# Kernel tuning notes

Hardware: AMD Instinct MI355X
Metric: run time of the kernel (lower is better)

Reference implementation:

```python
import jax, jax.numpy as jnp
import numpy as np

IMG = 800          # original image H = W
OUT = 7            # pooled output size
SR = 2             # sampling_ratio
CANON_S = 224.0    # canonical_scale
CANON_L = 4.0      # canonical_level
EPS = 1e-6
KMIN, KMAX = 2, 5  # -log2 of first/last scale


def _bilinear_gather(feat, b_idx, y, x):
    """feat: [B,C,H,W]; b_idx: [N] int; y,x: [N,S] float sample coords.
    Returns [N,S,C]. Faithful to torchvision roi_align bilinear_interpolate
    (aligned=False semantics)."""
    B, C, H, W = feat.shape
    valid = (y > -1.0) & (y < H) & (x > -1.0) & (x < W)
    y = jnp.clip(y, 0.0, None)
    x = jnp.clip(x, 0.0, None)
    yl = jnp.minimum(jnp.floor(y).astype(jnp.int32), H - 1)
    xl = jnp.minimum(jnp.floor(x).astype(jnp.int32), W - 1)
    yh = jnp.minimum(yl + 1, H - 1)
    xh = jnp.minimum(xl + 1, W - 1)
    y = jnp.where(yl >= H - 1, yl.astype(y.dtype), y)
    x = jnp.where(xl >= W - 1, xl.astype(x.dtype), x)
    ly = y - yl
    lx = x - xl
    hy = 1.0 - ly
    hx = 1.0 - lx
    flat = feat.transpose(0, 2, 3, 1).reshape(B * H * W, C)  # [B*H*W, C]
    base = b_idx[:, None] * (H * W)                            # [N,1]

    def g(yy, xx):
        return flat[base + yy * W + xx]  # gather -> [N,S,C]

    val = ((hy * hx)[..., None] * g(yl, xl)
           + (hy * lx)[..., None] * g(yl, xh)
           + (ly * hx)[..., None] * g(yh, xl)
           + (ly * lx)[..., None] * g(yh, xh))
    return jnp.where(valid[..., None], val, 0.0)


def _roi_align(feat, rois, scale):
    """Single-level RoIAlign, aligned=False. rois: [N,5] = (batch_idx,x1,y1,x2,y2)."""
    N = rois.shape[0]
    C = feat.shape[1]
    b_idx = rois[:, 0].astype(jnp.int32)
    x1 = rois[:, 1] * scale
    y1 = rois[:, 2] * scale
    x2 = rois[:, 3] * scale
    y2 = rois[:, 4] * scale
    roi_w = jnp.maximum(x2 - x1, 1.0)
    roi_h = jnp.maximum(y2 - y1, 1.0)
    bin_w = roi_w / OUT
    bin_h = roi_h / OUT
    # sample offsets within the roi, in units of bins: [OUT*SR]
    off = (jnp.arange(OUT, dtype=feat.dtype)[:, None]
           + (jnp.arange(SR, dtype=feat.dtype)[None, :] + 0.5) / SR).reshape(-1)
    ys = y1[:, None] + off[None, :] * bin_h[:, None]  # [N, OUT*SR]
    xs = x1[:, None] + off[None, :] * bin_w[:, None]  # [N, OUT*SR]
    S = OUT * SR
    Y = jnp.broadcast_to(ys[:, :, None], (N, S, S)).reshape(N, S * S)
    X = jnp.broadcast_to(xs[:, None, :], (N, S, S)).reshape(N, S * S)
    val = _bilinear_gather(feat, b_idx, Y, X)          # [N, S*S, C]
    val = val.reshape(N, OUT, SR, OUT, SR, C).mean(axis=(2, 4))  # avg over samples
    return val.transpose(0, 3, 1, 2)                   # [N, C, OUT, OUT]


def setup_inputs() -> dict:
    key = jax.random.key(0)
    ks = jax.random.split(key, 7)
    feats = {}
    for i, hw in enumerate([200, 100, 50, 25]):
        feats[f"feat{i}"] = jax.random.normal(ks[i], (2, 256, hw, hw), dtype=jnp.float32)
    # boxes [2, 256, 4] in (x1,y1,x2,y2), sizes log-uniform in [16, ~590] px
    xy1 = jax.random.uniform(ks[4], (2, 256, 2), minval=0.0, maxval=IMG - 32.0)
    sz = 2.0 ** jax.random.uniform(ks[5], (2, 256, 2), minval=4.0, maxval=9.2)
    xy2 = jnp.minimum(xy1 + sz, float(IMG))
    boxes = jnp.concatenate([xy1, xy2], axis=-1).astype(jnp.float32)
    return {**feats, "boxes": boxes}


def reference(feat0, feat1, feat2, feat3, boxes):
    feats = [feat0, feat1, feat2, feat3]
    # _infer_scale: round(log2(feat_size / image_size)) -> power-of-two scale
    scales = [2.0 ** round(float(np.log2(f.shape[2] / IMG))) for f in feats]
    # _convert_to_roi_format
    B, Nb, _ = boxes.shape
    ids = jnp.repeat(jnp.arange(B, dtype=boxes.dtype), Nb)[:, None]
    rois = jnp.concatenate([ids, boxes.reshape(B * Nb, 4)], axis=1)  # [N,5]
    # LevelMapper (FPN eq.1)
    s = jnp.sqrt((rois[:, 3] - rois[:, 1]) * (rois[:, 4] - rois[:, 2]))
    lvls = jnp.floor(CANON_L + jnp.log2(s / CANON_S) + EPS)
    lvls = jnp.clip(lvls, KMIN, KMAX).astype(jnp.int32) - KMIN  # [N] in {0..3}
    out = jnp.zeros((B * Nb, feat0.shape[1], OUT, OUT), dtype=feat0.dtype)
    for lvl, (f, sc) in enumerate(zip(feats, scales)):
        r = _roi_align(f, rois, sc)
        out = jnp.where((lvls == lvl)[:, None, None, None], r, out)
    return out
```

## Files before the change

kernel.cpp:

```cpp
#include <hip/hip_runtime.h>
#include <hip/hip_bf16.h>


#define IMGC   256
#define OUTP   7
#define NBIN   49
#define SAMP   14
#define BT     128
#define TLD    132
#define SLD    68

#define WS_O1 20480000
#define WS_O2 25600000
#define WS_O3 26880000
#define WS_TOT 27200000

__global__ __launch_bounds__(256) void transpose_cl_kernel(
    const float* __restrict__ f0, const float* __restrict__ f1,
    const float* __restrict__ f2, const float* __restrict__ f3,
    float* __restrict__ ws)
{
    __shared__ float t[64 * SLD];

    int bx = blockIdx.x;
    int lvl, r;
    if (bx < 5000)      { lvl = 0; r = bx; }
    else if (bx < 6256) { lvl = 1; r = bx - 5000; }
    else if (bx < 6576) { lvl = 2; r = bx - 6256; }
    else                { lvl = 3; r = bx - 6576; }

    const int  Mtab[4]  = {40000, 10000, 2500, 625};
    const int  Mttab[4] = {625, 157, 40, 10};
    const int  wsoff[4] = {0, WS_O1, WS_O2, WS_O3};

    const float* in = (lvl == 0) ? f0 : (lvl == 1) ? f1 : (lvl == 2) ? f2 : f3;
    float* outp = ws + wsoff[lvl];
    const int M  = Mtab[lvl];
    const int Mt = Mttab[lvl];

    int mt   = r % Mt;
    int rest = r / Mt;
    int ct   = rest & 3;
    int bb   = rest >> 2;
    int m0   = mt * 64;

    const bool vec = (m0 + 64 <= M) && ((M & 3) == 0);

    if (vec) {
        int mq = threadIdx.x & 15;
        int cg = threadIdx.x >> 4;
        const float* ibase = in + (bb * IMGC + ct * 64) * M + m0;
        #pragma unroll
        for (int j = 0; j < 4; ++j) {
            int c = cg + 16 * j;
            float4 v = *(const float4*)(ibase + c * M + 4 * mq);
            *(float4*)&t[c * SLD + 4 * mq] = v;
        }
        __syncthreads();
        int cq = threadIdx.x & 15;
        int mr = threadIdx.x >> 4;
        float* obase = outp + (bb * M + m0) * IMGC + ct * 64;
        #pragma unroll
        for (int j = 0; j < 4; ++j) {
            int m = mr + 16 * j;
            float4 v;
            v.x = t[(4 * cq + 0) * SLD + m];
            v.y = t[(4 * cq + 1) * SLD + m];
            v.z = t[(4 * cq + 2) * SLD + m];
            v.w = t[(4 * cq + 3) * SLD + m];
            *(float4*)(obase + m * IMGC + 4 * cq) = v;
        }
    } else {
        int tx = threadIdx.x & 63;
        int tg = threadIdx.x >> 6;
        {
            int m = m0 + tx;
            if (m < M) {
                int base = (bb * IMGC + ct * 64) * M + m;
                #pragma unroll
                for (int k = 0; k < 16; ++k) {
                    int cc = tg * 16 + k;
                    t[cc * SLD + tx] = in[base + cc * M];
                }
            }
        }
        __syncthreads();
        #pragma unroll
        for (int k = 0; k < 16; ++k) {
            int mm = tg * 16 + k;
            int m = m0 + mm;
            if (m < M)
                outp[(bb * M + m) * IMGC + ct * 64 + tx] = t[tx * SLD + mm];
        }
    }
}

__global__ __launch_bounds__(BT) void roialign_cl_kernel(
    const float* __restrict__ f0, const float* __restrict__ f1,
    const float* __restrict__ f2, const float* __restrict__ f3,
    const float* __restrict__ boxes, float* __restrict__ out)
{
    __shared__ float  s_ly[SAMP], s_wy[SAMP], s_lx[SAMP], s_wx[SAMP];
    __shared__ int    s_yol[SAMP], s_yoh[SAMP], s_xol[SAMP], s_xoh[SAMP];
    __shared__ float4 s_w[SAMP * SAMP];
    __shared__ float  tile[NBIN * TLD];

    const int tid = threadIdx.x;
    const int blk = blockIdx.x;
    const int n   = blk >> 1;
    const int c0  = (blk & 1) * BT;
    const int b   = n >> 8;

    const float x1 = boxes[n * 4 + 0];
    const float y1 = boxes[n * 4 + 1];
    const float x2 = boxes[n * 4 + 2];
    const float y2 = boxes[n * 4 + 3];

    float s = sqrtf(fmaxf((x2 - x1) * (y2 - y1), 1e-12f));
    float lf = floorf(4.0f + log2f(s / 224.0f) + 1e-6f);
    int lvl = (int)fminf(fmaxf(lf, 2.0f), 5.0f) - 2;

    const int   Htab[4]  = {200, 100, 50, 25};
    const float sctab[4] = {0.25f, 0.125f, 0.0625f, 0.03125f};
    const int   H = Htab[lvl];
    const int   W = H;
    const float scale = sctab[lvl];
    const float* fp = (lvl == 0) ? f0 : (lvl == 1) ? f1 : (lvl == 2) ? f2 : f3;

    const float x1s = x1 * scale, y1s = y1 * scale;
    const float roi_w = fmaxf(x2 * scale - x1s, 1.0f);
    const float roi_h = fmaxf(y2 * scale - y1s, 1.0f);
    const float bin_w = roi_w * (1.0f / OUTP);
    const float bin_h = roi_h * (1.0f / OUTP);

    if (tid < SAMP) {
        int t = tid;
        float off = (float)(t >> 1) + 0.25f + 0.5f * (float)(t & 1);
        float y = y1s + off * bin_h;
        float v = (y > -1.0f && y < (float)H) ? 1.0f : 0.0f;
        y = fmaxf(y, 0.0f);
        int yl = min((int)y, H - 1);
        int yh = min(yl + 1, H - 1);
        if (yl >= H - 1) y = (float)yl;
        s_ly[t] = y - (float)yl;
        s_wy[t] = v;
        s_yol[t] = ((b * H + yl) * W) * (IMGC / 4);
        s_yoh[t] = ((b * H + yh) * W) * (IMGC / 4);
    } else if (tid >= 64 && tid < 64 + SAMP) {
        int t = tid - 64;
        float off = (float)(t >> 1) + 0.25f + 0.5f * (float)(t & 1);
        float x = x1s + off * bin_w;
        float v = (x > -1.0f && x < (float)W) ? 1.0f : 0.0f;
        x = fmaxf(x, 0.0f);
        int xl = min((int)x, W - 1);
        int xh = min(xl + 1, W - 1);
        if (xl >= W - 1) x = (float)xl;
        s_lx[t] = x - (float)xl;
        s_wx[t] = v;
        s_xol[t] = xl * (IMGC / 4);
        s_xoh[t] = xh * (IMGC / 4);
    }
    __syncthreads();

    for (int idx = tid; idx < SAMP * SAMP; idx += BT) {
        int i = idx / SAMP;
        int j = idx - i * SAMP;
        float v  = s_wy[i] * s_wx[j] * 0.25f;
        float ly = s_ly[i], lx = s_lx[j];
        float hy = 1.0f - ly, hx = 1.0f - lx;
        float4 w;
        w.x = v * hy * hx;
        w.y = v * hy * lx;
        w.z = v * ly * hx;
        w.w = v * ly * lx;
        s_w[idx] = w;
    }
    __syncthreads();

    const int quad = tid & 31;
    const int bg   = tid >> 5;
    const float4* fp4 = (const float4*)fp + (c0 / 4) + quad;

    for (int bin = bg; bin < NBIN; bin += 4) {
        int ph = bin / OUTP;
        int pw = bin - ph * OUTP;
        float4 acc; acc.x = acc.y = acc.z = acc.w = 0.0f;
        #pragma unroll
        for (int sy = 0; sy < 2; ++sy) {
            #pragma unroll
            for (int sx = 0; sx < 2; ++sx) {
                int i = 2 * ph + sy;
                int j = 2 * pw + sx;
                float4 w = s_w[i * SAMP + j];
                int yol = s_yol[i], yoh = s_yoh[i];
                int xol = s_xol[j], xoh = s_xoh[j];
                float4 v1 = fp4[yol + xol];
                float4 v2 = fp4[yol + xoh];
                float4 v3 = fp4[yoh + xol];
                float4 v4 = fp4[yoh + xoh];
                acc.x += w.x * v1.x + w.y * v2.x + w.z * v3.x + w.w * v4.x;
                acc.y += w.x * v1.y + w.y * v2.y + w.z * v3.y + w.w * v4.y;
                acc.z += w.x * v1.z + w.y * v2.z + w.z * v3.z + w.w * v4.z;
                acc.w += w.x * v1.w + w.y * v2.w + w.z * v3.w + w.w * v4.w;
            }
        }
        *(float4*)&tile[bin * TLD + 4 * quad] = acc;
    }
    __syncthreads();

    const int outbase = n * (IMGC * NBIN) + c0 * NBIN;
    for (int t = tid; t < BT * NBIN; t += BT) {
        int cl = t / NBIN;
        int bb = t - cl * NBIN;
        out[outbase + t] = tile[bb * TLD + cl];
    }
}

__global__ __launch_bounds__(BT) void roialign_direct_kernel(
    const float* __restrict__ f0, const float* __restrict__ f1,
    const float* __restrict__ f2, const float* __restrict__ f3,
    const float* __restrict__ boxes, float* __restrict__ out)
{
    __shared__ float s_ly[SAMP], s_wy[SAMP], s_lx[SAMP], s_wx[SAMP];
    __shared__ int   s_yol[SAMP], s_yoh[SAMP], s_xol[SAMP], s_xoh[SAMP];
    __shared__ float tile[NBIN * (BT + 1)];

    const int tid = threadIdx.x;
    const int blk = blockIdx.x;
    const int n   = blk >> 1;
    const int c0  = (blk & 1) * BT;
    const int b   = n >> 8;

    const float x1 = boxes[n * 4 + 0];
    const float y1 = boxes[n * 4 + 1];
    const float x2 = boxes[n * 4 + 2];
    const float y2 = boxes[n * 4 + 3];

    float s = sqrtf(fmaxf((x2 - x1) * (y2 - y1), 1e-12f));
    float lf = floorf(4.0f + log2f(s / 224.0f) + 1e-6f);
    int lvl = (int)fminf(fmaxf(lf, 2.0f), 5.0f) - 2;

    const int   Htab[4]  = {200, 100, 50, 25};
    const float sctab[4] = {0.25f, 0.125f, 0.0625f, 0.03125f};
    const int   H = Htab[lvl];
    const int   W = H;
    const float scale = sctab[lvl];
    const float* fp = (lvl == 0) ? f0 : (lvl == 1) ? f1 : (lvl == 2) ? f2 : f3;

    const float x1s = x1 * scale, y1s = y1 * scale;
    const float roi_w = fmaxf(x2 * scale - x1s, 1.0f);
    const float roi_h = fmaxf(y2 * scale - y1s, 1.0f);
    const float bin_w = roi_w * (1.0f / OUTP);
    const float bin_h = roi_h * (1.0f / OUTP);

    if (tid < SAMP) {
        int t = tid;
        float off = (float)(t >> 1) + 0.25f + 0.5f * (float)(t & 1);
        float y = y1s + off * bin_h;
        float v = (y > -1.0f && y < (float)H) ? 1.0f : 0.0f;
        y = fmaxf(y, 0.0f);
        int yl = min((int)y, H - 1);
        int yh = min(yl + 1, H - 1);
        if (yl >= H - 1) y = (float)yl;
        s_ly[t] = y - (float)yl;
        s_wy[t] = v;
        s_yol[t] = yl * W; s_yoh[t] = yh * W;
    } else if (tid >= 64 && tid < 64 + SAMP) {
        int t = tid - 64;
        float off = (float)(t >> 1) + 0.25f + 0.5f * (float)(t & 1);
        float x = x1s + off * bin_w;
        float v = (x > -1.0f && x < (float)W) ? 1.0f : 0.0f;
        x = fmaxf(x, 0.0f);
        int xl = min((int)x, W - 1);
        int xh = min(xl + 1, W - 1);
        if (xl >= W - 1) x = (float)xl;
        s_lx[t] = x - (float)xl;
        s_wx[t] = v;
        s_xol[t] = xl; s_xoh[t] = xh;
    }
    __syncthreads();

    const int c  = c0 + tid;
    const int tb = (b * IMGC + c) * (H * W);

    for (int bin = 0; bin < NBIN; ++bin) {
        int ph = bin / OUTP;
        int pw = bin - ph * OUTP;
        float acc = 0.0f;
        #pragma unroll
        for (int sy = 0; sy < 2; ++sy) {
            #pragma unroll
            for (int sx = 0; sx < 2; ++sx) {
                int i = 2 * ph + sy;
                int j = 2 * pw + sx;
                float ly = s_ly[i], lx = s_lx[j];
                float hy = 1.0f - ly, hx = 1.0f - lx;
                float wm = s_wy[i] * s_wx[j];
                float v1 = fp[tb + s_yol[i] + s_xol[j]];
                float v2 = fp[tb + s_yol[i] + s_xoh[j]];
                float v3 = fp[tb + s_yoh[i] + s_xol[j]];
                float v4 = fp[tb + s_yoh[i] + s_xoh[j]];
                acc += wm * (hy * (hx * v1 + lx * v2) + ly * (hx * v3 + lx * v4));
            }
        }
        tile[bin * (BT + 1) + tid] = acc * 0.25f;
    }
    __syncthreads();

    const int outbase = n * (IMGC * NBIN) + c0 * NBIN;
    for (int t = tid; t < BT * NBIN; t += BT) {
        int cl = t / NBIN;
        int bb = t - cl * NBIN;
        out[outbase + t] = tile[bb * (BT + 1) + cl];
    }
}

extern "C" void kernel_launch(void* const* d_in, const int* in_sizes, int n_in,
                              void* d_out, int out_size, void* d_ws, size_t ws_size,
                              hipStream_t stream) {
    const float* f0    = (const float*)d_in[0];
    const float* f1    = (const float*)d_in[1];
    const float* f2    = (const float*)d_in[2];
    const float* f3    = (const float*)d_in[3];
    const float* boxes = (const float*)d_in[4];
    float* out = (float*)d_out;

    const bool use_cl = ws_size >= (size_t)WS_TOT * sizeof(float);

    if (use_cl) {
        float* w = (float*)d_ws;
        transpose_cl_kernel<<<6656, 256, 0, stream>>>(f0, f1, f2, f3, w);
        roialign_cl_kernel<<<1024, BT, 0, stream>>>(
            w, w + WS_O1, w + WS_O2, w + WS_O3, boxes, out);
    } else {
        roialign_direct_kernel<<<1024, BT, 0, stream>>>(f0, f1, f2, f3, boxes, out);
    }
}
```

Before: 198.1 us.

## Store channels-last workspace in fp16 and gather half8 vectors in RoIAlign

The transpose kernel now writes the channels-last copy of each feature level as _Float16 instead of float. Each block handles all 256 channels of a 64-pixel tile through a larger, padded shared buffer with scalar loads. The RoIAlign kernel gathers half8 vectors, converts them to float and accumulates in fp32. This halves workspace write and gather traffic, at the cost of fp16 rounding of the features, which may exceed the accuracy tolerance. The transpose input reads are now scalar rather than float4.

```diff
diff --git a/kernel.cpp b/kernel.cpp
--- a/kernel.cpp
+++ b/kernel.cpp
@@ -8,97 +8,77 @@
 #define SAMP   14
 #define BT     128
 #define TLD    132
-#define SLD    68
+#define SLD    65
 
 #define WS_O1 20480000
 #define WS_O2 25600000
 #define WS_O3 26880000
 #define WS_TOT 27200000
 
-__global__ __launch_bounds__(256) void transpose_cl_kernel(
+typedef _Float16 half2v __attribute__((ext_vector_type(2)));
+typedef _Float16 half8  __attribute__((ext_vector_type(8)));
+
+__global__ __launch_bounds__(256) void transpose_cl_h_kernel(
     const float* __restrict__ f0, const float* __restrict__ f1,
     const float* __restrict__ f2, const float* __restrict__ f3,
-    float* __restrict__ ws)
+    _Float16* __restrict__ ws)
 {
-    __shared__ float t[64 * SLD];
+    __shared__ float t[IMGC * SLD];
 
     int bx = blockIdx.x;
     int lvl, r;
-    if (bx < 5000)      { lvl = 0; r = bx; }
-    else if (bx < 6256) { lvl = 1; r = bx - 5000; }
-    else if (bx < 6576) { lvl = 2; r = bx - 6256; }
-    else                { lvl = 3; r = bx - 6576; }
-
-    const int  Mtab[4]  = {40000, 10000, 2500, 625};
-    const int  Mttab[4] = {625, 157, 40, 10};
-    const int  wsoff[4] = {0, WS_O1, WS_O2, WS_O3};
+    if (bx < 1250)      { lvl = 0; r = bx; }
+    else if (bx < 1564) { lvl = 1; r = bx - 1250; }
+    else if (bx < 1644) { lvl = 2; r = bx - 1564; }
+    else                { lvl = 3; r = bx - 1644; }
+
+    const int Mtab[4]  = {40000, 10000, 2500, 625};
+    const int Mttab[4] = {625, 157, 40, 10};
+    const int wsoff[4] = {0, WS_O1, WS_O2, WS_O3};
 
     const float* in = (lvl == 0) ? f0 : (lvl == 1) ? f1 : (lvl == 2) ? f2 : f3;
-    float* outp = ws + wsoff[lvl];
+    _Float16* outp = ws + wsoff[lvl];
     const int M  = Mtab[lvl];
     const int Mt = Mttab[lvl];
 
-    int mt   = r % Mt;
-    int rest = r / Mt;
-    int ct   = rest & 3;
-    int bb   = rest >> 2;
-    int m0   = mt * 64;
-
-    const bool vec = (m0 + 64 <= M) && ((M & 3) == 0);
-
-    if (vec) {
-        int mq = threadIdx.x & 15;
-        int cg = threadIdx.x >> 4;
-        const float* ibase = in + (bb * IMGC + ct * 64) * M + m0;
-        #pragma unroll
-        for (int j = 0; j < 4; ++j) {
-            int c = cg + 16 * j;
-            float4 v = *(const float4*)(ibase + c * M + 4 * mq);
-            *(float4*)&t[c * SLD + 4 * mq] = v;
-        }
-        __syncthreads();
-        int cq = threadIdx.x & 15;
-        int mr = threadIdx.x >> 4;
-        float* obase = outp + (bb * M + m0) * IMGC + ct * 64;
-        #pragma unroll
-        for (int j = 0; j < 4; ++j) {
-            int m = mr + 16 * j;
-            float4 v;
-            v.x = t[(4 * cq + 0) * SLD + m];
-            v.y = t[(4 * cq + 1) * SLD + m];
-            v.z = t[(4 * cq + 2) * SLD + m];
-            v.w = t[(4 * cq + 3) * SLD + m];
-            *(float4*)(obase + m * IMGC + 4 * cq) = v;
-        }
-    } else {
-        int tx = threadIdx.x & 63;
-        int tg = threadIdx.x >> 6;
-        {
-            int m = m0 + tx;
-            if (m < M) {
-                int base = (bb * IMGC + ct * 64) * M + m;
-                #pragma unroll
-                for (int k = 0; k < 16; ++k) {
-                    int cc = tg * 16 + k;
-                    t[cc * SLD + tx] = in[base + cc * M];
-                }
+    int mt = r % Mt;
+    int bb = r / Mt;
+    int m0 = mt * 64;
+
+    const int tid = threadIdx.x;
+    const int tx  = tid & 63;
+    const int tg  = tid >> 6;
+
+    {
+        int m = m0 + tx;
+        if (m < M) {
+            const float* base = in + (size_t)(bb * IMGC + tg * 64) * M + m;
+            #pragma unroll
+            for (int k = 0; k < 64; ++k) {
+                t[(tg * 64 + k) * SLD + tx] = base[(size_t)k * M];
             }
         }
-        __syncthreads();
-        #pragma unroll
-        for (int k = 0; k < 16; ++k) {
-            int mm = tg * 16 + k;
-            int m = m0 + mm;
-            if (m < M)
-                outp[(bb * M + m) * IMGC + ct * 64 + tx] = t[tx * SLD + mm];
+    }
+    __syncthreads();
+
+    #pragma unroll
+    for (int k = 0; k < 32; ++k) {
+        int idx = tid + 256 * k;
+        int mm  = idx >> 7;
+        int cp  = idx & 127;
+        int m2  = m0 + mm;
+        if (m2 < M) {
+            float a = t[(2 * cp) * SLD + mm];
+            float b = t[(2 * cp + 1) * SLD + mm];
+            half2v h; h.x = (_Float16)a; h.y = (_Float16)b;
+            *(half2v*)&outp[(size_t)(bb * M + m2) * IMGC + 2 * cp] = h;
         }
     }
 }
 
-__global__ __launch_bounds__(BT) void roialign_cl_kernel(
-    const float* __restrict__ f0, const float* __restrict__ f1,
-    const float* __restrict__ f2, const float* __restrict__ f3,
-    const float* __restrict__ boxes, float* __restrict__ out)
+__global__ __launch_bounds__(BT) void roialign_h_kernel(
+    const _Float16* __restrict__ ws, const float* __restrict__ boxes,
+    float* __restrict__ out)
 {
     __shared__ float  s_ly[SAMP], s_wy[SAMP], s_lx[SAMP], s_wx[SAMP];
     __shared__ int    s_yol[SAMP], s_yoh[SAMP], s_xol[SAMP], s_xoh[SAMP];
@@ -120,12 +100,13 @@
     float lf = floorf(4.0f + log2f(s / 224.0f) + 1e-6f);
     int lvl = (int)fminf(fmaxf(lf, 2.0f), 5.0f) - 2;
 
-    const int   Htab[4]  = {200, 100, 50, 25};
-    const float sctab[4] = {0.25f, 0.125f, 0.0625f, 0.03125f};
+    const int   Htab[4]   = {200, 100, 50, 25};
+    const float sctab[4]  = {0.25f, 0.125f, 0.0625f, 0.03125f};
+    const int   wsoff[4]  = {0, WS_O1, WS_O2, WS_O3};
     const int   H = Htab[lvl];
     const int   W = H;
     const float scale = sctab[lvl];
-    const float* fp = (lvl == 0) ? f0 : (lvl == 1) ? f1 : (lvl == 2) ? f2 : f3;
+    const _Float16* fp = ws + wsoff[lvl];
 
     const float x1s = x1 * scale, y1s = y1 * scale;
     const float roi_w = fmaxf(x2 * scale - x1s, 1.0f);
@@ -144,8 +125,8 @@
         if (yl >= H - 1) y = (float)yl;
         s_ly[t] = y - (float)yl;
         s_wy[t] = v;
-        s_yol[t] = ((b * H + yl) * W) * (IMGC / 4);
-        s_yoh[t] = ((b * H + yh) * W) * (IMGC / 4);
+        s_yol[t] = ((b * H + yl) * W) * (IMGC / 8);
+        s_yoh[t] = ((b * H + yh) * W) * (IMGC / 8);
     } else if (tid >= 64 && tid < 64 + SAMP) {
         int t = tid - 64;
         float off = (float)(t >> 1) + 0.25f + 0.5f * (float)(t & 1);
@@ -157,8 +138,8 @@
         if (xl >= W - 1) x = (float)xl;
         s_lx[t] = x - (float)xl;
         s_wx[t] = v;
-        s_xol[t] = xl * (IMGC / 4);
-        s_xoh[t] = xh * (IMGC / 4);
+        s_xol[t] = xl * (IMGC / 8);
+        s_xoh[t] = xh * (IMGC / 8);
     }
     __syncthreads();
 
@@ -177,14 +158,16 @@
     }
     __syncthreads();
 
-    const int quad = tid & 31;
-    const int bg   = tid >> 5;
-    const float4* fp4 = (const float4*)fp + (c0 / 4) + quad;
-
-    for (int bin = bg; bin < NBIN; bin += 4) {
+    const int o  = tid & 15;
+    const int bg = tid >> 4;
+    const half8* fb = (const half8*)fp + (c0 >> 3) + o;
+
+    for (int bin = bg; bin < NBIN; bin += 8) {
         int ph = bin / OUTP;
         int pw = bin - ph * OUTP;
-        float4 acc; acc.x = acc.y = acc.z = acc.w = 0.0f;
+        float acc[8];
+        #pragma unroll
+        for (int k = 0; k < 8; ++k) acc[k] = 0.0f;
         #pragma unroll
         for (int sy = 0; sy < 2; ++sy) {
             #pragma unroll
@@ -194,17 +177,20 @@
                 float4 w = s_w[i * SAMP + j];
                 int yol = s_yol[i], yoh = s_yoh[i];
                 int xol = s_xol[j], xoh = s_xoh[j];
-                float4 v1 = fp4[yol + xol];
-                float4 v2 = fp4[yol + xoh];
-                float4 v3 = fp4[yoh + xol];
-                float4 v4 = fp4[yoh + xoh];
-                acc.x += w.x * v1.x + w.y * v2.x + w.z * v3.x + w.w * v4.x;
-                acc.y += w.x * v1.y + w.y * v2.y + w.z * v3.y + w.w * v4.y;
-                acc.z += w.x * v1.z + w.y * v2.z + w.z * v3.z + w.w * v4.z;
-                acc.w += w.x * v1.w + w.y * v2.w + w.z * v3.w + w.w * v4.w;
+                half8 v1 = fb[yol + xol];
+                half8 v2 = fb[yol + xoh];
+                half8 v3 = fb[yoh + xol];
+                half8 v4 = fb[yoh + xoh];
+                #pragma unroll
+                for (int k = 0; k < 8; ++k) {
+                    acc[k] += w.x * (float)v1[k] + w.y * (float)v2[k]
+                            + w.z * (float)v3[k] + w.w * (float)v4[k];
+                }
             }
         }
-        *(float4*)&tile[bin * TLD + 4 * quad] = acc;
+        float* tp = &tile[bin * TLD + 8 * o];
+        *(float4*)(tp + 0) = make_float4(acc[0], acc[1], acc[2], acc[3]);
+        *(float4*)(tp + 4) = make_float4(acc[4], acc[5], acc[6], acc[7]);
     }
     __syncthreads();
 
@@ -325,13 +311,12 @@
     const float* boxes = (const float*)d_in[4];
     float* out = (float*)d_out;
 
-    const bool use_cl = ws_size >= (size_t)WS_TOT * sizeof(float);
+    const bool use_cl = ws_size >= (size_t)WS_TOT * sizeof(_Float16);
 
     if (use_cl) {
-        float* w = (float*)d_ws;
-        transpose_cl_kernel<<<6656, 256, 0, stream>>>(f0, f1, f2, f3, w);
-        roialign_cl_kernel<<<1024, BT, 0, stream>>>(
-            w, w + WS_O1, w + WS_O2, w + WS_O3, boxes, out);
+        _Float16* w = (_Float16*)d_ws;
+        transpose_cl_h_kernel<<<1664, 256, 0, stream>>>(f0, f1, f2, f3, w);
+        roialign_h_kernel<<<1024, BT, 0, stream>>>(w, boxes, out);
     } else {
         roialign_direct_kernel<<<1024, BT, 0, stream>>>(f0, f1, f2, f3, boxes, out);
     }
```

Result: faster. 181.2 us (-8.5%).
